# Kernel optimization log

Measured on AMD Instinct MI355X. Metric: run time of the kernel, lower is better.

## Reference

```python
import jax, jax.numpy as jnp
import numpy as np

B, S, F, H = 2, 2048, 1024, 16
HD = F // H


def setup_inputs() -> dict:
    key = jax.random.key(0)
    ks = jax.random.split(key, 9)
    Q = jax.random.normal(ks[0], (B, S, F), dtype=jnp.float32)
    K = jax.random.normal(ks[1], (B, S, F), dtype=jnp.float32)
    V = jax.random.normal(ks[2], (B, S, F), dtype=jnp.float32)
    # additive pre-softmax causal mask: 0 on/below diagonal, -1e9 above
    causal = jnp.tril(jnp.ones((S, S), dtype=bool))
    mask_1 = jnp.where(causal, 0.0, -1e9).astype(jnp.float32)[None, None]
    # multiplicative post-softmax mask in [0,1)
    mask_2 = jax.random.uniform(ks[3], (1, 1, S, S), dtype=jnp.float32)
    scale = 1.0 / np.sqrt(F)
    W_q = jax.random.normal(ks[4], (F, F), dtype=jnp.float32) * scale
    W_k = jax.random.normal(ks[5], (F, F), dtype=jnp.float32) * scale
    W_v = jax.random.normal(ks[6], (F, F), dtype=jnp.float32) * scale
    W_o = jax.random.normal(ks[7], (F, F), dtype=jnp.float32) * scale
    return {"Q": Q, "K": K, "V": V, "mask_1": mask_1, "mask_2": mask_2,
            "W_q": W_q, "W_k": W_k, "W_v": W_v, "W_o": W_o}


def reference(Q, K, V, mask_1, mask_2, W_q, W_k, W_v, W_o):
    # Linear projections (no bias), split into heads: [B,S,F] -> [B,H,S,HD]
    def proj(x, W):
        return (x @ W.T).reshape(B, S, H, HD).transpose(0, 2, 1, 3)
    q, k, v = proj(Q, W_q), proj(K, W_k), proj(V, W_v)
    # scores [B,H,S,S], scaled by sqrt(head_size)
    scores = jnp.einsum('bhqd,bhkd->bhqk', q, k) / np.sqrt(HD)
    scores = scores + mask_1  # additive pre-softmax mask
    probs = jax.nn.softmax(scores, axis=-1) * mask_2  # multiplicative post-softmax mask
    out = jnp.einsum('bhqk,bhkd->bhqd', probs, v)
    out = out.transpose(0, 2, 1, 3).reshape(B, S, F)
    return out @ W_o.T
```

## Files before the change

kernel.cpp:

```cpp
#include <hip/hip_runtime.h>
#include <hip/hip_bf16.h>
#include <stdint.h>

typedef __bf16 bf16_t;
typedef __bf16 bf16x8 __attribute__((ext_vector_type(8)));
typedef __bf16 bf16x4v __attribute__((ext_vector_type(4)));
typedef float f32x4 __attribute__((ext_vector_type(4)));

#define GLDS16(g, l)                                                         \
  __builtin_amdgcn_global_load_lds(                                          \
      (const __attribute__((address_space(1))) void*)(g),                    \
      (__attribute__((address_space(3))) void*)(l), 16, 0, 0)

__device__ __forceinline__ f32x4 mfma16(bf16x8 a, bf16x8 b, f32x4 c) {
  return __builtin_amdgcn_mfma_f32_16x16x32_bf16(a, b, c, 0, 0, 0);
}

static constexpr int S = 2048, F = 1024, H = 16, HD = 64;

static constexpr size_t OFF_QB  = 0;
static constexpr size_t OFF_KB  = 4194304;
static constexpr size_t OFF_VB  = 8388608;
static constexpr size_t OFF_WQ  = 12582912;
static constexpr size_t OFF_WK  = 13631488;
static constexpr size_t OFF_WV  = 14680064;
static constexpr size_t OFF_WO  = 15728640;
static constexpr size_t OFF_QP  = 16777216;
static constexpr size_t OFF_KP  = 20971520;
static constexpr size_t OFF_VPT = 25165824;
static constexpr size_t OFF_M2  = 29360128;
static constexpr size_t OFF_ATT = 0;

__global__ void cvt_all(const float* __restrict__ s0, const float* __restrict__ s1,
                        const float* __restrict__ s2, const float* __restrict__ s3,
                        const float* __restrict__ w0, const float* __restrict__ w1,
                        const float* __restrict__ w2, const float* __restrict__ w3,
                        bf16_t* __restrict__ d0, bf16_t* __restrict__ d1,
                        bf16_t* __restrict__ d2, bf16_t* __restrict__ d3,
                        bf16_t* __restrict__ e0, bf16_t* __restrict__ e1,
                        bf16_t* __restrict__ e2, bf16_t* __restrict__ e3) {
  const float* s;
  bf16_t* d;
  size_t r;
  if (blockIdx.x < 8192) {
    int t = blockIdx.x * 256 + threadIdx.x;
    int a = t >> 19;
    r = (size_t)(t & 0x7FFFF) * 8;
    s = (a == 0) ? s0 : (a == 1) ? s1 : (a == 2) ? s2 : s3;
    d = (a == 0) ? d0 : (a == 1) ? d1 : (a == 2) ? d2 : d3;
  } else {
    int t = (blockIdx.x - 8192) * 256 + threadIdx.x;
    int a = t >> 17;
    r = (size_t)(t & 0x1FFFF) * 8;
    s = (a == 0) ? w0 : (a == 1) ? w1 : (a == 2) ? w2 : w3;
    d = (a == 0) ? e0 : (a == 1) ? e1 : (a == 2) ? e2 : e3;
  }
  const float4* sp = (const float4*)(s + r);
  float4 u = sp[0], v = sp[1];
  bf16x8 o;
  o[0] = (bf16_t)u.x; o[1] = (bf16_t)u.y; o[2] = (bf16_t)u.z; o[3] = (bf16_t)u.w;
  o[4] = (bf16_t)v.x; o[5] = (bf16_t)v.y; o[6] = (bf16_t)v.z; o[7] = (bf16_t)v.w;
  *(bf16x8*)(d + r) = o;
}

__device__ __forceinline__ void stage128x32(const bf16_t* __restrict__ g, int ld,
                                            bf16_t* lds, int wv, int ln) {
#pragma unroll
  for (int i = 0; i < 2; ++i) {
    int ch  = wv * 2 + i;
    int row = ch * 16 + (ln >> 2);
    int col = (ln & 3) * 8;
    GLDS16(g + (size_t)row * ld + col, lds + ch * 512);
  }
}

__global__ __launch_bounds__(256, 2) void proj_gemm(
    const bf16_t* __restrict__ Qb, const bf16_t* __restrict__ Kb, const bf16_t* __restrict__ Vb,
    const bf16_t* __restrict__ Wq, const bf16_t* __restrict__ Wk, const bf16_t* __restrict__ Wv,
    bf16_t* __restrict__ qp, bf16_t* __restrict__ kp, bf16_t* __restrict__ vpT) {
  __shared__ bf16_t As[2][128 * 32];
  __shared__ bf16_t Bs[2][128 * 32];
  const int z = blockIdx.z;
  const bf16_t* A = (z == 0) ? Qb : (z == 1) ? Kb : Vb;
  const bf16_t* W = (z == 0) ? Wq : (z == 1) ? Wk : Wv;
  const int m0 = blockIdx.x * 128, n0 = blockIdx.y * 128;
  const int tid = threadIdx.x, wv = tid >> 6, ln = tid & 63;
  const int wr = wv >> 1, wc = wv & 1, lr = ln & 15, lg = ln >> 4;
  f32x4 acc[4][4];
#pragma unroll
  for (int i = 0; i < 4; ++i)
#pragma unroll
    for (int j = 0; j < 4; ++j) acc[i][j] = (f32x4){0.f, 0.f, 0.f, 0.f};

  stage128x32(A + (size_t)m0 * F, F, As[0], wv, ln);
  stage128x32(W + (size_t)n0 * F, F, Bs[0], wv, ln);
  __syncthreads();

  for (int k0 = 0; k0 < F; k0 += 32) {
    const int cur = (k0 >> 5) & 1;
    if (k0 + 32 < F) {
      stage128x32(A + (size_t)m0 * F + k0 + 32, F, As[cur ^ 1], wv, ln);
      stage128x32(W + (size_t)n0 * F + k0 + 32, F, Bs[cur ^ 1], wv, ln);
    }
    bf16x8 af[4], bfr[4];
#pragma unroll
    for (int i = 0; i < 4; ++i)
      af[i] = *(const bf16x8*)&As[cur][(wr * 64 + i * 16 + lr) * 32 + lg * 8];
#pragma unroll
    for (int j = 0; j < 4; ++j)
      bfr[j] = *(const bf16x8*)&Bs[cur][(wc * 64 + j * 16 + lr) * 32 + lg * 8];
#pragma unroll
    for (int i = 0; i < 4; ++i)
#pragma unroll
      for (int j = 0; j < 4; ++j) acc[i][j] = mfma16(af[i], bfr[j], acc[i][j]);
    __syncthreads();
  }

  const int rbase = m0 + wr * 64, cbase = n0 + wc * 64;
  if (z < 2) {
    bf16_t* out = (z == 0) ? qp : kp;
    const float qscl = (z == 0) ? 0.18033688f : 1.0f;
#pragma unroll
    for (int i = 0; i < 4; ++i)
#pragma unroll
      for (int j = 0; j < 4; ++j) {
        int r0 = rbase + i * 16 + lg * 4;
        int c  = cbase + j * 16 + lr;
        int b = r0 >> 11, s = r0 & 2047, h = c >> 6, d = c & 63;
        size_t base = ((size_t)(b * H + h) * S + s) * HD + d;
#pragma unroll
        for (int reg = 0; reg < 4; ++reg)
          out[base + (size_t)reg * HD] = (bf16_t)(acc[i][j][reg] * qscl);
      }
  } else {
#pragma unroll
    for (int i = 0; i < 4; ++i)
#pragma unroll
      for (int j = 0; j < 4; ++j) {
        int r0 = rbase + i * 16 + lg * 4;
        int c  = cbase + j * 16 + lr;
        int b = r0 >> 11, s = r0 & 2047, h = c >> 6, d = c & 63;
        size_t base = ((size_t)(b * H + h) * HD + d) * S + s;
        bf16x4v pv;
#pragma unroll
        for (int reg = 0; reg < 4; ++reg) pv[reg] = (bf16_t)acc[i][j][reg];
        *(bf16x4v*)&vpT[base] = pv;
      }
  }
}

__global__ __launch_bounds__(256, 2) void out_gemm(
    const bf16_t* __restrict__ A, const bf16_t* __restrict__ W, float* __restrict__ out) {
  __shared__ bf16_t As[2][128 * 32];
  __shared__ bf16_t Bs[2][128 * 32];
  const int m0 = blockIdx.x * 128, n0 = blockIdx.y * 128;
  const int tid = threadIdx.x, wv = tid >> 6, ln = tid & 63;
  const int wr = wv >> 1, wc = wv & 1, lr = ln & 15, lg = ln >> 4;
  f32x4 acc[4][4];
#pragma unroll
  for (int i = 0; i < 4; ++i)
#pragma unroll
    for (int j = 0; j < 4; ++j) acc[i][j] = (f32x4){0.f, 0.f, 0.f, 0.f};

  stage128x32(A + (size_t)m0 * F, F, As[0], wv, ln);
  stage128x32(W + (size_t)n0 * F, F, Bs[0], wv, ln);
  __syncthreads();

  for (int k0 = 0; k0 < F; k0 += 32) {
    const int cur = (k0 >> 5) & 1;
    if (k0 + 32 < F) {
      stage128x32(A + (size_t)m0 * F + k0 + 32, F, As[cur ^ 1], wv, ln);
      stage128x32(W + (size_t)n0 * F + k0 + 32, F, Bs[cur ^ 1], wv, ln);
    }
    bf16x8 af[4], bfr[4];
#pragma unroll
    for (int i = 0; i < 4; ++i)
      af[i] = *(const bf16x8*)&As[cur][(wr * 64 + i * 16 + lr) * 32 + lg * 8];
#pragma unroll
    for (int j = 0; j < 4; ++j)
      bfr[j] = *(const bf16x8*)&Bs[cur][(wc * 64 + j * 16 + lr) * 32 + lg * 8];
#pragma unroll
    for (int i = 0; i < 4; ++i)
#pragma unroll
      for (int j = 0; j < 4; ++j) acc[i][j] = mfma16(af[i], bfr[j], acc[i][j]);
    __syncthreads();
  }
#pragma unroll
  for (int i = 0; i < 4; ++i)
#pragma unroll
    for (int j = 0; j < 4; ++j) {
      int r0 = m0 + wr * 64 + i * 16 + lg * 4;
      int c  = n0 + wc * 64 + j * 16 + lr;
#pragma unroll
      for (int reg = 0; reg < 4; ++reg)
        out[(size_t)(r0 + reg) * F + c] = acc[i][j][reg];
    }
}

__global__ __launch_bounds__(256, 4) void flash(
    const bf16_t* __restrict__ qp, const bf16_t* __restrict__ kp,
    const bf16_t* __restrict__ vpT, const bf16_t* __restrict__ m2b,
    bf16_t* __restrict__ PA, bf16_t* __restrict__ PB,
    float* __restrict__ lA, float* __restrict__ lB) {
  __shared__ bf16_t Ks[2][64 * 64];
  __shared__ bf16_t Vs[2][64 * 64];
  const int ur = blockIdx.x >> 5, bh = blockIdx.x & 31;
  const int grp = ur / 3, rem = ur % 3;
  int qt, kvlo, kvhi;
  if (rem == 2) { qt = 15 - grp; kvlo = 0; kvhi = qt; }
  else {
    qt = 31 - grp;
    int half = (qt + 2) >> 1;
    if (rem == 0) { kvlo = 0; kvhi = half - 1; }
    else          { kvlo = half; kvhi = qt; }
  }
  bf16_t* __restrict__ PO = (rem == 1) ? PB : PA;
  float*  __restrict__ LO = (rem == 1) ? lB : lA;

  const int tid = threadIdx.x, wv = tid >> 6, ln = tid & 63;
  const int lr = ln & 15, lg = ln >> 4;
  const bf16_t* qb = qp + (size_t)bh * S * HD;
  const bf16_t* kb = kp + (size_t)bh * S * HD;
  const bf16_t* vb = vpT + (size_t)bh * HD * S;
  const int q0w = qt * 64 + wv * 16;
  const int qg  = q0w + lr;

  bf16x8 bq[2];
#pragma unroll
  for (int h2 = 0; h2 < 2; ++h2)
    bq[h2] = *(const bf16x8*)&qb[(size_t)qg * HD + h2 * 32 + lg * 8];

  float ls = 0.f;
  f32x4 accv[4];
#pragma unroll
  for (int n = 0; n < 4; ++n) accv[n] = (f32x4){0.f, 0.f, 0.f, 0.f};

  const int srow0 = ln >> 3, scc0 = ln & 7;
  const int pxor = lr & 7;

#pragma unroll
  for (int i = 0; i < 2; ++i) {
    int ch = wv * 2 + i;
    int row = ch * 8 + srow0;
    int scc = scc0 ^ (row & 7);
    GLDS16(kb + (size_t)(kvlo * 64 + row) * HD + scc * 8, Ks[0] + ch * 512);
    GLDS16(vb + (size_t)row * S + kvlo * 64 + scc * 8, Vs[0] + ch * 512);
  }
  __syncthreads();

  for (int kt = kvlo; kt <= kvhi; ++kt) {
    const int k0 = kt * 64;
    const int cur = (kt - kvlo) & 1;

    bf16x4v m2v[4];
#pragma unroll
    for (int c = 0; c < 4; ++c)
      m2v[c] = *(const bf16x4v*)&m2b[(size_t)qg * S + k0 + c * 16 + lg * 4];

    if (kt < kvhi) {
      const int kn = k0 + 64;
#pragma unroll
      for (int i = 0; i < 2; ++i) {
        int ch = wv * 2 + i;
        int row = ch * 8 + srow0;
        int scc = scc0 ^ (row & 7);
        GLDS16(kb + (size_t)(kn + row) * HD + scc * 8, Ks[cur ^ 1] + ch * 512);
        GLDS16(vb + (size_t)row * S + kn + scc * 8, Vs[cur ^ 1] + ch * 512);
      }
    }

    f32x4 st[4];
    __builtin_amdgcn_s_setprio(1);
#pragma unroll
    for (int c = 0; c < 4; ++c) {
      int kr = c * 16 + lr;
      int sw = kr & 7;
      bf16x8 ak0 = *(const bf16x8*)&Ks[cur][kr * 64 + ((lg ^ sw) * 8)];
      bf16x8 ak1 = *(const bf16x8*)&Ks[cur][kr * 64 + (((4 + lg) ^ sw) * 8)];
      f32x4 t = (f32x4){0.f, 0.f, 0.f, 0.f};
      t = mfma16(ak0, bq[0], t);
      t = mfma16(ak1, bq[1], t);
      st[c] = t;
    }
    __builtin_amdgcn_s_setprio(0);
    if (kt == qt) {
#pragma unroll
      for (int c = 0; c < 4; ++c)
#pragma unroll
        for (int r = 0; r < 4; ++r) {
          int kgl = k0 + c * 16 + lg * 4 + r;
          if (kgl > qg) st[c][r] = -1e30f;
        }
    }
    bf16x4v pw[4];
#pragma unroll
    for (int c = 0; c < 4; ++c) {
      float p0 = exp2f(st[c][0]), p1 = exp2f(st[c][1]);
      float p2 = exp2f(st[c][2]), p3 = exp2f(st[c][3]);
      ls += (p0 + p1) + (p2 + p3);
      pw[c][0] = (bf16_t)(p0 * (float)m2v[c][0]);
      pw[c][1] = (bf16_t)(p1 * (float)m2v[c][1]);
      pw[c][2] = (bf16_t)(p2 * (float)m2v[c][2]);
      pw[c][3] = (bf16_t)(p3 * (float)m2v[c][3]);
    }
    asm volatile("s_barrier" ::: "memory");
    bf16_t* Pw = &Ks[cur][wv * 1024];
#pragma unroll
    for (int c = 0; c < 4; ++c) {
      int chunk = (2 * c + (lg >> 1)) ^ pxor;
      *(bf16x4v*)&Pw[lr * 64 + chunk * 8 + (lg & 1) * 4] = pw[c];
    }
    __builtin_amdgcn_s_setprio(1);
#pragma unroll
    for (int kc = 0; kc < 2; ++kc) {
      int pchunk = (4 * kc + lg) ^ pxor;
      bf16x8 pb = *(const bf16x8*)&Pw[lr * 64 + pchunk * 8];
#pragma unroll
      for (int n = 0; n < 4; ++n) {
        int dr = n * 16 + lr;
        int sw = dr & 7;
        bf16x8 av = *(const bf16x8*)&Vs[cur][dr * 64 + (((kc * 4 + lg) ^ sw) * 8)];
        accv[n] = mfma16(av, pb, accv[n]);
      }
    }
    __builtin_amdgcn_s_setprio(0);
    __syncthreads();
  }

  ls += __shfl_xor(ls, 16, 64);
  ls += __shfl_xor(ls, 32, 64);
  if (lg == 0) LO[bh * S + qg] = ls;
#pragma unroll
  for (int n = 0; n < 4; ++n) {
    bf16x4v ov;
#pragma unroll
    for (int r = 0; r < 4; ++r) ov[r] = (bf16_t)accv[n][r];
    *(bf16x4v*)&PO[((size_t)bh * S + qg) * HD + n * 16 + lg * 4] = ov;
  }
}

__global__ void norm_cvt(const bf16_t* __restrict__ PA, const bf16_t* __restrict__ PB,
                         const float* __restrict__ lA, const float* __restrict__ lB,
                         bf16_t* __restrict__ att) {
  int t = blockIdx.x * 256 + threadIdx.x;
  int bh = t >> 13;
  int rm = t & 8191;
  int s  = rm >> 2;
  int d0 = (rm & 3) * 16;
  size_t pbase = ((size_t)bh * S + s) * HD + d0;
  bf16x8 a0 = *(const bf16x8*)&PA[pbase];
  bf16x8 a1 = *(const bf16x8*)&PA[pbase + 8];
  float l = lA[bh * S + s];
  float o[16];
#pragma unroll
  for (int i = 0; i < 8; ++i) { o[i] = (float)a0[i]; o[8 + i] = (float)a1[i]; }
  if (s >= 1024) {
    bf16x8 b0 = *(const bf16x8*)&PB[pbase];
    bf16x8 b1 = *(const bf16x8*)&PB[pbase + 8];
    l += lB[bh * S + s];
#pragma unroll
    for (int i = 0; i < 8; ++i) { o[i] += (float)b0[i]; o[8 + i] += (float)b1[i]; }
  }
  float inv = 1.0f / l;
  int b = bh >> 4, h = bh & 15;
  bf16x8 w0, w1;
#pragma unroll
  for (int i = 0; i < 8; ++i) {
    w0[i] = (bf16_t)(o[i] * inv);
    w1[i] = (bf16_t)(o[8 + i] * inv);
  }
  size_t obase = ((size_t)(b * S + s)) * F + h * HD + d0;
  *(bf16x8*)&att[obase] = w0;
  *(bf16x8*)&att[obase + 8] = w1;
}

extern "C" void kernel_launch(void* const* d_in, const int* in_sizes, int n_in,
                              void* d_out, int out_size, void* d_ws, size_t ws_size,
                              hipStream_t stream) {
  (void)in_sizes; (void)n_in; (void)out_size; (void)ws_size;
  const float* Q  = (const float*)d_in[0];
  const float* K  = (const float*)d_in[1];
  const float* V  = (const float*)d_in[2];
  const float* M2 = (const float*)d_in[4];
  const float* Wq = (const float*)d_in[5];
  const float* Wk = (const float*)d_in[6];
  const float* Wv = (const float*)d_in[7];
  const float* Wo = (const float*)d_in[8];
  bf16_t* ws = (bf16_t*)d_ws;

  bf16_t *Qb = ws + OFF_QB, *Kb = ws + OFF_KB, *Vb = ws + OFF_VB;
  bf16_t *WqB = ws + OFF_WQ, *WkB = ws + OFF_WK, *WvB = ws + OFF_WV, *WoB = ws + OFF_WO;
  bf16_t *qpB = ws + OFF_QP, *kpB = ws + OFF_KP, *vpT = ws + OFF_VPT;
  bf16_t *m2b = ws + OFF_M2, *att = ws + OFF_ATT;
  bf16_t *PA = ws + OFF_KB, *PB = ws + OFF_VB;
  float  *lA = (float*)(ws + OFF_WQ), *lB = (float*)(ws + OFF_WK);

  cvt_all<<<10240, 256, 0, stream>>>(Q, K, V, M2, Wq, Wk, Wv, Wo,
                                     Qb, Kb, Vb, m2b, WqB, WkB, WvB, WoB);
  proj_gemm<<<dim3(32, 8, 3), 256, 0, stream>>>(Qb, Kb, Vb, WqB, WkB, WvB, qpB, kpB, vpT);
  flash<<<dim3(1536), 256, 0, stream>>>(qpB, kpB, vpT, m2b, PA, PB, lA, lB);
  norm_cvt<<<1024, 256, 0, stream>>>(PA, PB, lA, lB, att);
  out_gemm<<<dim3(32, 8), 256, 0, stream>>>(att, WoB, (float*)d_out);
}
```

Before: 138.1 us.

## Split causal flash work into up to three KV partitions via lookup table

Replaces the two-way KV split of the flash kernel with a constant table of 60 work units per head. Each unit carries its own q tile, KV range and partial-output slot, and long rows are split into up to three partials. The goal is better load balancing across the 1920 blocks, ordered longest first. In exchange it needs a third partial buffer and extra merge reads in norm_cvt, and the attention output moves to a different workspace region.

Result: faster. 133.2 us (median of 2 runs) (-3.5%).

```diff
diff --git a/kernel.cpp b/kernel.cpp
--- a/kernel.cpp
+++ b/kernel.cpp
@@ -29,7 +29,25 @@
 static constexpr size_t OFF_KP  = 20971520;
 static constexpr size_t OFF_VPT = 25165824;
 static constexpr size_t OFF_M2  = 29360128;
-static constexpr size_t OFF_ATT = 0;
+
+__device__ __constant__ uint32_t UNIT_TBL[60] = {
+  0x000B000Bu, 0x0016000Bu, 0x0017000Bu, 0x01170C17u,
+  0x000A000Au, 0x0014000Au, 0x0015000Au, 0x01150B15u,
+  0x01160C16u, 0x001E000Au, 0x001F000Au, 0x011F0B15u,
+  0x00090009u, 0x00120009u, 0x00130009u, 0x01130A13u,
+  0x01140B14u, 0x001B0009u, 0x001C0009u, 0x011C0A13u,
+  0x001D0009u, 0x011D0A13u, 0x021D141Du, 0x011E0B14u,
+  0x021E151Eu, 0x021F161Fu,
+  0x00080008u, 0x00100008u, 0x00110008u, 0x01110911u,
+  0x01120A12u, 0x00180008u, 0x00190008u, 0x01190911u,
+  0x001A0008u, 0x011A0911u, 0x021A121Au, 0x011B0A12u,
+  0x021B131Bu, 0x021C141Cu,
+  0x00070007u, 0x000E0007u, 0x000F0007u, 0x010F080Fu,
+  0x01100910u, 0x01180910u, 0x02181118u, 0x02191219u,
+  0x00060006u, 0x000C0006u, 0x000D0006u, 0x010D070Du, 0x010E080Eu,
+  0x00050005u, 0x010C070Cu,
+  0x00040004u, 0x00030003u, 0x00020002u, 0x00010001u, 0x00000000u
+};
 
 __global__ void cvt_all(const float* __restrict__ s0, const float* __restrict__ s1,
                         const float* __restrict__ s2, const float* __restrict__ s3,
@@ -200,22 +218,16 @@
 __global__ __launch_bounds__(256, 4) void flash(
     const bf16_t* __restrict__ qp, const bf16_t* __restrict__ kp,
     const bf16_t* __restrict__ vpT, const bf16_t* __restrict__ m2b,
-    bf16_t* __restrict__ PA, bf16_t* __restrict__ PB,
-    float* __restrict__ lA, float* __restrict__ lB) {
+    bf16_t* __restrict__ PA, bf16_t* __restrict__ PB, bf16_t* __restrict__ PC,
+    float* __restrict__ lA, float* __restrict__ lB, float* __restrict__ lC) {
   __shared__ bf16_t Ks[2][64 * 64];
   __shared__ bf16_t Vs[2][64 * 64];
   const int ur = blockIdx.x >> 5, bh = blockIdx.x & 31;
-  const int grp = ur / 3, rem = ur % 3;
-  int qt, kvlo, kvhi;
-  if (rem == 2) { qt = 15 - grp; kvlo = 0; kvhi = qt; }
-  else {
-    qt = 31 - grp;
-    int half = (qt + 2) >> 1;
-    if (rem == 0) { kvlo = 0; kvhi = half - 1; }
-    else          { kvlo = half; kvhi = qt; }
-  }
-  bf16_t* __restrict__ PO = (rem == 1) ? PB : PA;
-  float*  __restrict__ LO = (rem == 1) ? lB : lA;
+  const uint32_t e = UNIT_TBL[ur];
+  const int kvhi = e & 0xFF, kvlo = (e >> 8) & 0xFF;
+  const int qt = (e >> 16) & 0xFF, part = (int)(e >> 24);
+  bf16_t* __restrict__ PO = (part == 0) ? PA : (part == 1) ? PB : PC;
+  float*  __restrict__ LO = (part == 0) ? lA : (part == 1) ? lB : lC;
 
   const int tid = threadIdx.x, wv = tid >> 6, ln = tid & 63;
   const int lr = ln & 15, lg = ln >> 4;
@@ -340,8 +352,9 @@
 }
 
 __global__ void norm_cvt(const bf16_t* __restrict__ PA, const bf16_t* __restrict__ PB,
+                         const bf16_t* __restrict__ PC,
                          const float* __restrict__ lA, const float* __restrict__ lB,
-                         bf16_t* __restrict__ att) {
+                         const float* __restrict__ lC, bf16_t* __restrict__ att) {
   int t = blockIdx.x * 256 + threadIdx.x;
   int bh = t >> 13;
   int rm = t & 8191;
@@ -354,12 +367,19 @@
   float o[16];
 #pragma unroll
   for (int i = 0; i < 8; ++i) { o[i] = (float)a0[i]; o[8 + i] = (float)a1[i]; }
-  if (s >= 1024) {
+  if (s >= 768) {
     bf16x8 b0 = *(const bf16x8*)&PB[pbase];
     bf16x8 b1 = *(const bf16x8*)&PB[pbase + 8];
     l += lB[bh * S + s];
 #pragma unroll
     for (int i = 0; i < 8; ++i) { o[i] += (float)b0[i]; o[8 + i] += (float)b1[i]; }
+  }
+  if (s >= 1536) {
+    bf16x8 c0 = *(const bf16x8*)&PC[pbase];
+    bf16x8 c1 = *(const bf16x8*)&PC[pbase + 8];
+    l += lC[bh * S + s];
+#pragma unroll
+    for (int i = 0; i < 8; ++i) { o[i] += (float)c0[i]; o[8 + i] += (float)c1[i]; }
   }
   float inv = 1.0f / l;
   int b = bh >> 4, h = bh & 15;
@@ -391,14 +411,16 @@
   bf16_t *Qb = ws + OFF_QB, *Kb = ws + OFF_KB, *Vb = ws + OFF_VB;
   bf16_t *WqB = ws + OFF_WQ, *WkB = ws + OFF_WK, *WvB = ws + OFF_WV, *WoB = ws + OFF_WO;
   bf16_t *qpB = ws + OFF_QP, *kpB = ws + OFF_KP, *vpT = ws + OFF_VPT;
-  bf16_t *m2b = ws + OFF_M2, *att = ws + OFF_ATT;
-  bf16_t *PA = ws + OFF_KB, *PB = ws + OFF_VB;
+  bf16_t *m2b = ws + OFF_M2;
+  bf16_t *PA = ws + OFF_KB, *PB = ws + OFF_VB, *PC = ws + OFF_QB;
   float  *lA = (float*)(ws + OFF_WQ), *lB = (float*)(ws + OFF_WK);
+  float  *lC = (float*)(ws + OFF_WV);
+  bf16_t *att = ws + OFF_QP;
 
   cvt_all<<<10240, 256, 0, stream>>>(Q, K, V, M2, Wq, Wk, Wv, Wo,
                                      Qb, Kb, Vb, m2b, WqB, WkB, WvB, WoB);
   proj_gemm<<<dim3(32, 8, 3), 256, 0, stream>>>(Qb, Kb, Vb, WqB, WkB, WvB, qpB, kpB, vpT);
-  flash<<<dim3(1536), 256, 0, stream>>>(qpB, kpB, vpT, m2b, PA, PB, lA, lB);
-  norm_cvt<<<1024, 256, 0, stream>>>(PA, PB, lA, lB, att);
+  flash<<<dim3(1920), 256, 0, stream>>>(qpB, kpB, vpT, m2b, PA, PB, PC, lA, lB, lC);
+  norm_cvt<<<1024, 256, 0, stream>>>(PA, PB, PC, lA, lB, lC, att);
   out_gemm<<<dim3(32, 8), 256, 0, stream>>>(att, WoB, (float*)d_out);
 }
```
